# Kernel optimization log

Measured on AMD Instinct MI355X. Metric: run time of the kernel, lower is better.

## Reference

```python
import jax, jax.numpy as jnp
import numpy as np

N_STORE, N_DEPT, F_IN = 100_000, 20_000, 128
E = 1_000_000
H, C = 4, 16  # heads, per-head channels; hidden = H*C = 64
NUM_LAYERS = 3


def setup_inputs() -> dict:
    key = jax.random.key(0)
    ks = jax.random.split(key, 16)
    def edges(k, n_src, n_dst):
        k1, k2 = jax.random.split(k)
        src = jax.random.randint(k1, (E,), 0, n_src, dtype=jnp.int32)
        dst = jax.random.randint(k2, (E,), 0, n_dst, dtype=jnp.int32)
        return jnp.stack([src, dst])
    s = 0.05
    return {
        "x_store": jax.random.normal(ks[0], (N_STORE, F_IN), jnp.float32),
        "x_dept": jax.random.normal(ks[1], (N_DEPT, F_IN), jnp.float32),
        "edge_sd": edges(ks[2], N_STORE, N_DEPT),   # store -> dept
        "edge_ds": edges(ks[3], N_DEPT, N_STORE),   # dept  -> store
        "edge_ss": edges(ks[4], N_STORE, N_STORE),  # store -> store
        "W_src0": jax.random.normal(ks[5], (3, F_IN, H * C), jnp.float32) * s,
        "W_dst0": jax.random.normal(ks[6], (3, F_IN, H * C), jnp.float32) * s,
        "W_src_h": jax.random.normal(ks[7], (2, 3, H * C, H * C), jnp.float32) * s,
        "W_dst_h": jax.random.normal(ks[8], (2, 3, H * C, H * C), jnp.float32) * s,
        "att_src": jax.random.normal(ks[9], (3, 3, H, C), jnp.float32) * s,
        "att_dst": jax.random.normal(ks[10], (3, 3, H, C), jnp.float32) * s,
        "bias": jnp.zeros((3, 3, H * C), jnp.float32),
    }


def gat_conv(x_src, x_dst, edge, W_s, W_d, a_s, a_d, b, n_dst):
    """PyG GATConv, bipartite, add_self_loops=False, eval mode (no dropout)."""
    h_s = (x_src @ W_s).reshape(-1, H, C)   # [N_src, H, C]
    h_d = (x_dst @ W_d).reshape(-1, H, C)   # [N_dst, H, C]
    al_s = jnp.sum(h_s * a_s, axis=-1)      # [N_src, H]
    al_d = jnp.sum(h_d * a_d, axis=-1)      # [N_dst, H]
    src, dst = edge[0], edge[1]
    e = jax.nn.leaky_relu(al_s[src] + al_d[dst], 0.2)        # [E, H]
    m = jax.ops.segment_max(e, dst, num_segments=n_dst)       # segment softmax
    m = jnp.where(jnp.isfinite(m), m, 0.0)
    ex = jnp.exp(e - m[dst])
    denom = jax.ops.segment_sum(ex, dst, num_segments=n_dst)
    alpha = ex / (denom[dst] + 1e-16)                          # [E, H]
    msg = h_s[src] * alpha[:, :, None]                         # [E, H, C]
    out = jax.ops.segment_sum(msg, dst, num_segments=n_dst)    # [N_dst, H, C]
    return out.reshape(n_dst, H * C) + b


def _forward(x_store, x_dept, edge_sd, edge_ds, edge_ss,
             W_src0, W_dst0, W_src_h, W_dst_h, att_src, att_dst, bias):
    xs, xd = x_store, x_dept
    for i in range(NUM_LAYERS):
        Ws = W_src0 if i == 0 else W_src_h[i - 1]
        Wd = W_dst0 if i == 0 else W_dst_h[i - 1]
        # edge type 0: store->dept ; 1: dept->store ; 2: store->store
        o_dept = gat_conv(xs, xd, edge_sd, Ws[0], Wd[0], att_src[i, 0], att_dst[i, 0], bias[i, 0], N_DEPT)
        o1 = gat_conv(xd, xs, edge_ds, Ws[1], Wd[1], att_src[i, 1], att_dst[i, 1], bias[i, 1], N_STORE)
        o2 = gat_conv(xs, xs, edge_ss, Ws[2], Wd[2], att_src[i, 2], att_dst[i, 2], bias[i, 2], N_STORE)
        o_store = (o1 + o2) * 0.5  # HeteroConv aggr='mean' across relations into 'store'
        if i < NUM_LAYERS - 1:
            xs, xd = jax.nn.relu(o_store), jax.nn.relu(o_dept)  # dropout is identity in eval
        else:
            xs, xd = o_store, o_dept
    return jnp.concatenate([xs, xd], axis=0)  # [N_STORE + N_DEPT, 64]


def reference(x_store, x_dept, edge_sd, edge_ds, edge_ss,
              W_src0, W_dst0, W_src_h, W_dst_h, att_src, att_dst, bias):
    return _forward(x_store, x_dept, edge_sd, edge_ds, edge_ss,
                    W_src0, W_dst0, W_src_h, W_dst_h, att_src, att_dst, bias)
```

## Files before the change

kernel.cpp:

```cpp
#include <hip/hip_runtime.h>
#include <hip/hip_bf16.h>

#define N_STORE 100000
#define N_DEPT  20000
#define F_IN    128
#define NTOT    (N_DEPT + 2 * N_STORE)

#define NB0   157
#define NB12  196
#define NBUCK (NB0 + 2 * NB12)

using u16    = unsigned short;
using bf16x8 = __attribute__((ext_vector_type(8))) __bf16;
using f32x4  = __attribute__((ext_vector_type(4))) float;

__device__ __forceinline__ float b2f(u16 x) {
    unsigned u = ((unsigned)x) << 16;
    return __builtin_bit_cast(float, u);
}
__device__ __forceinline__ u16 f2b(float f) {
    unsigned u = __builtin_bit_cast(unsigned, f);
    u += 0x7FFFu + ((u >> 16) & 1u);
    return (u16)(u >> 16);
}

__global__ void k_zeroi(int* p, int n) {
    int i = blockIdx.x * 256 + threadIdx.x;
    if (i < n) p[i] = 0;
}

__global__ void k_bcount(const int* __restrict__ e0, const int* __restrict__ e1,
                         const int* __restrict__ e2, int E, int* __restrict__ bucketCnt) {
    __shared__ int c[256];
    int t = threadIdx.x;
    c[t] = 0; __syncthreads();
    int rel = blockIdx.y;
    const int* e = (rel == 0) ? e0 : (rel == 1) ? e1 : e2;
    int n = (rel == 0) ? N_DEPT : N_STORE;
    int shift = (rel == 0) ? 7 : 9;
    int i0 = blockIdx.x * 2048 + t;
#pragma unroll
    for (int k = 0; k < 8; ++k) {
        int i = i0 + k * 256;
        if (i < E) {
            int d = e[E + i];
            if ((unsigned)d < (unsigned)n) atomicAdd(&c[d >> shift], 1);
        }
    }
    __syncthreads();
    int bbase = (rel == 0) ? 0 : (rel == 1) ? NB0 : NB0 + NB12;
    int nb = (rel == 0) ? NB0 : NB12;
    if (t < nb && c[t]) atomicAdd(&bucketCnt[bbase + t], c[t]);
}

__global__ void k_bscan(const int* __restrict__ bucketCnt, int* __restrict__ bucketOfs,
                        int* __restrict__ bucketCur, int* __restrict__ offs) {
    __shared__ int s[1024];
    int t = threadIdx.x;
    int v = (t < NBUCK) ? bucketCnt[t] : 0;
    s[t] = v; __syncthreads();
    for (int o = 1; o < 1024; o <<= 1) {
        int u = (t >= o) ? s[t - o] : 0;
        __syncthreads();
        s[t] += u;
        __syncthreads();
    }
    if (t < NBUCK) {
        bucketOfs[t + 1] = s[t];
        bucketCur[t] = s[t] - v;
    }
    if (t == 0) bucketOfs[0] = 0;
    if (t == NBUCK - 1) offs[NTOT] = s[t];
}

__global__ void k_bscatter(const int* __restrict__ e0, const int* __restrict__ e1,
                           const int* __restrict__ e2, int E,
                           int* __restrict__ bucketCur, unsigned* __restrict__ pairs) {
    __shared__ int c[256];
    __shared__ int base[256];
    int t = threadIdx.x;
    c[t] = 0; __syncthreads();
    int rel = blockIdx.y;
    const int* e = (rel == 0) ? e0 : (rel == 1) ? e1 : e2;
    int n = (rel == 0) ? N_DEPT : N_STORE;
    int shift = (rel == 0) ? 7 : 9;
    int i0 = blockIdx.x * 2048 + t;
    int mb[8], mr[8]; unsigned mv[8];
#pragma unroll
    for (int k = 0; k < 8; ++k) {
        int i = i0 + k * 256;
        mb[k] = -1;
        if (i < E) {
            int d = e[E + i];
            if ((unsigned)d < (unsigned)n) {
                int b = d >> shift;
                mb[k] = b;
                mr[k] = atomicAdd(&c[b], 1);
                mv[k] = (unsigned)e[i] | ((unsigned)(d - (b << shift)) << 20);
            }
        }
    }
    __syncthreads();
    int bbase = (rel == 0) ? 0 : (rel == 1) ? NB0 : NB0 + NB12;
    int nb = (rel == 0) ? NB0 : NB12;
    if (t < nb && c[t]) base[t] = atomicAdd(&bucketCur[bbase + t], c[t]);
    __syncthreads();
#pragma unroll
    for (int k = 0; k < 8; ++k)
        if (mb[k] >= 0) pairs[base[mb[k]] + mr[k]] = mv[k];
}

__global__ void k_bfinal(const unsigned* __restrict__ pairs, const int* __restrict__ bucketOfs,
                         int* __restrict__ offs, int* __restrict__ srcs_all) {
    int b = blockIdx.x, t = threadIdx.x;
    int rel = (b < NB0) ? 0 : (b < NB0 + NB12) ? 1 : 2;
    int shift = (rel == 0) ? 7 : 9;
    int bLocal = b - ((rel == 0) ? 0 : (rel == 1) ? NB0 : NB0 + NB12);
    int n = (rel == 0) ? N_DEPT : N_STORE;
    int gbase = (rel == 0) ? 0 : (rel == 1) ? N_DEPT : N_DEPT + N_STORE;
    int nodeLo = bLocal << shift;
    int bsize = 1 << shift;
    int nNodes = n - nodeLo; if (nNodes > bsize) nNodes = bsize;
    int pairLo = bucketOfs[b], pairHi = bucketOfs[b + 1];
    __shared__ int cnt[512], sc[512];
    cnt[t] = 0; cnt[t + 256] = 0;
    __syncthreads();
    for (int p = pairLo + t; p < pairHi; p += 256)
        atomicAdd(&cnt[pairs[p] >> 20], 1);
    __syncthreads();
    sc[t] = cnt[t]; sc[t + 256] = cnt[t + 256];
    __syncthreads();
    for (int o = 1; o < 512; o <<= 1) {
        int a0 = (t >= o) ? sc[t - o] : 0;
        int a1 = (t + 256 >= o) ? sc[t + 256 - o] : 0;
        __syncthreads();
        sc[t] += a0; sc[t + 256] += a1;
        __syncthreads();
    }
    int ex0 = sc[t] - cnt[t];
    int ex1 = sc[t + 256] - cnt[t + 256];
    if (t < nNodes)       offs[gbase + nodeLo + t]       = pairLo + ex0;
    if (t + 256 < nNodes) offs[gbase + nodeLo + t + 256] = pairLo + ex1;
    __syncthreads();
    cnt[t] = ex0; cnt[t + 256] = ex1;
    __syncthreads();
    for (int p = pairLo + t; p < pairHi; p += 256) {
        unsigned u = pairs[p];
        int q = atomicAdd(&cnt[u >> 20], 1);
        srcs_all[pairLo + q] = (int)(u & 0xFFFFFu);
    }
}

__global__ void k_pack_store(const float* __restrict__ Wa, const float* __restrict__ Wb,
                             const float* __restrict__ Wd1, const float* __restrict__ Wd2,
                             const float* __restrict__ aS0, const float* __restrict__ aS2,
                             const float* __restrict__ aD1, const float* __restrict__ aD2,
                             int K, u16* __restrict__ out) {
    int id = blockIdx.x * 256 + threadIdx.x;
    int total = K * 144;
    if (id >= total) return;
    int k = id / 144, n = id - k * 144;
    float val;
    if (n < 64) val = Wa[k * 64 + n];
    else if (n < 128) val = Wb[k * 64 + (n - 64)];
    else {
        int g = (n - 128) >> 2, h = (n - 128) & 3;
        const float* W = (g == 0) ? Wa : (g == 1) ? Wb : (g == 2) ? Wd1 : Wd2;
        const float* a = (g == 0) ? aS0 : (g == 1) ? aS2 : (g == 2) ? aD1 : aD2;
        float acc = 0.f;
        for (int c = 0; c < 16; ++c) acc += W[k * 64 + h * 16 + c] * a[h * 16 + c];
        val = acc;
    }
    int KT = K >> 5;
    int ct = n >> 4, col = n & 15, kt = k >> 5, q = (k >> 3) & 3, j = k & 7;
    out[(size_t)((ct * KT + kt) * 64 + q * 16 + col) * 8 + j] = f2b(val);
}

__global__ void k_pack_dept(const float* __restrict__ Ws1, const float* __restrict__ Wd0,
                            const float* __restrict__ aD0, const float* __restrict__ aS1,
                            int K, u16* __restrict__ out) {
    int id = blockIdx.x * 256 + threadIdx.x;
    int total = K * 80;
    if (id >= total) return;
    int k = id / 80, n = id - k * 80;
    float val;
    if (n < 64) val = Ws1[k * 64 + n];
    else if (n < 72) {
        int g = (n - 64) >> 2, h = (n - 64) & 3;
        const float* W = g ? Ws1 : Wd0;
        const float* a = g ? aS1 : aD0;
        float acc = 0.f;
        for (int c = 0; c < 16; ++c) acc += W[k * 64 + h * 16 + c] * a[h * 16 + c];
        val = acc;
    } else val = 0.f;
    int KT = K >> 5;
    int ct = n >> 4, col = n & 15, kt = k >> 5, q = (k >> 3) & 3, j = k & 7;
    out[(size_t)((ct * KT + kt) * 64 + q * 16 + col) * 8 + j] = f2b(val);
}

template <int KT, int CVT, int MODE>
__global__ void k_gemm(const void* __restrict__ Ain, int nrows, int K,
                       const u16* __restrict__ Bpanel,
                       u16* __restrict__ H0, u16* __restrict__ H1,
                       u16* __restrict__ A0, u16* __restrict__ A1, u16* __restrict__ A2) {
    const int CT = (MODE == 0) ? 9 : 5;
    int wid = (blockIdx.x * blockDim.x + threadIdx.x) >> 6;
    int lane = threadIdx.x & 63;
    int m0 = wid << 4;
    if (m0 >= nrows) return;
    int r = lane & 15, q = lane >> 4;
    bf16x8 a[KT];
    if (CVT) {
        const float* ap = (const float*)Ain + (size_t)(m0 + r) * K + q * 8;
#pragma unroll
        for (int kt = 0; kt < KT; ++kt) {
            f32x4 f0 = *(const f32x4*)(ap + kt * 32);
            f32x4 f1 = *(const f32x4*)(ap + kt * 32 + 4);
            bf16x8 v;
#pragma unroll
            for (int j = 0; j < 4; ++j) {
                v[j]     = __builtin_bit_cast(__bf16, f2b(f0[j]));
                v[4 + j] = __builtin_bit_cast(__bf16, f2b(f1[j]));
            }
            a[kt] = v;
        }
    } else {
        const u16* ap = (const u16*)Ain + (size_t)(m0 + r) * K + q * 8;
#pragma unroll
        for (int kt = 0; kt < KT; ++kt) a[kt] = *(const bf16x8*)(ap + kt * 32);
    }
    const bf16x8* B = (const bf16x8*)Bpanel;
    int rowb = m0 + q * 4;
#pragma unroll
    for (int ct = 0; ct < CT; ++ct) {
        f32x4 acc = {0.f, 0.f, 0.f, 0.f};
#pragma unroll
        for (int kt = 0; kt < KT; ++kt)
            acc = __builtin_amdgcn_mfma_f32_16x16x32_bf16(a[kt], B[(ct * KT + kt) * 64 + lane], acc, 0, 0, 0);
        if (ct < 4) {
            u16* cp = H0 + (size_t)rowb * 64 + ct * 16 + r;
#pragma unroll
            for (int i = 0; i < 4; ++i) cp[(size_t)i * 64] = f2b(acc[i]);
        } else if (MODE == 0 && ct < 8) {
            u16* cp = H1 + (size_t)rowb * 64 + (ct - 4) * 16 + r;
#pragma unroll
            for (int i = 0; i < 4; ++i) cp[(size_t)i * 64] = f2b(acc[i]);
        } else {
            if (r < 4) {
                u16* cp = A0 + (size_t)rowb * 4 + r;
#pragma unroll
                for (int i = 0; i < 4; ++i) cp[(size_t)i * 4] = f2b(acc[i]);
            } else if (r < 8) {
                u16* cp = A1 + (size_t)rowb * 4 + (r - 4);
#pragma unroll
                for (int i = 0; i < 4; ++i) cp[(size_t)i * 4] = f2b(acc[i]);
            } else if (MODE == 0) {
                u16* cp = A2 + (size_t)rowb * 8 + (r - 8);
#pragma unroll
                for (int i = 0; i < 4; ++i) cp[(size_t)i * 8] = f2b(acc[i]);
            }
        }
    }
}

__device__ __forceinline__ float warp16_sum(float v) {
    v += __shfl_xor(v, 1);
    v += __shfl_xor(v, 2);
    v += __shfl_xor(v, 4);
    v += __shfl_xor(v, 8);
    return v;
}

__device__ __forceinline__ void agg_seg(const int* __restrict__ srcs, int j0, int j1, int nsrc,
                                        const u16* __restrict__ htab, const u16* __restrict__ altab,
                                        int lane, int slot, int h, int pbase, float ald,
                                        float& acc, float& den) {
    for (int j = j0; j < j1; j += 16) {
        int nb = j1 - j; if (nb > 16) nb = 16;
        int sv = srcs[j + (slot < nb ? slot : 0)];
        sv = ((unsigned)sv < (unsigned)nsrc) ? sv : 0;
        u16 avr = altab[(size_t)sv * 4 + h];
        float hv[16];
#pragma unroll
        for (int k = 0; k < 16; ++k) {
            int s = __builtin_amdgcn_readlane(sv, k);
            hv[k] = b2f(htab[(size_t)s * 64 + lane]);
        }
        float e = b2f(avr) + ald;
        e = (e > 0.f) ? e : 0.2f * e;
        float ex = (slot < nb) ? __expf(e) : 0.f;
        den += ex;
        int exi = __builtin_bit_cast(int, ex);
#pragma unroll
        for (int k = 0; k < 16; ++k) {
            float exv = __builtin_bit_cast(float,
                __builtin_amdgcn_ds_bpermute(pbase + (k << 2), exi));
            acc = fmaf(exv, hv[k], acc);
        }
    }
}

__global__ void __launch_bounds__(256) k_agg1(
                       const int* __restrict__ offs, const int* __restrict__ srcs,
                       const u16* __restrict__ hS0, const u16* __restrict__ alsS0,
                       const u16* __restrict__ aldD0,
                       const float* __restrict__ bias, int doRelu,
                       u16* __restrict__ bOut, float* __restrict__ fOut) {
    __shared__ float sAcc[4][64];
    __shared__ float sDen[4][64];
    int wl = threadIdx.x >> 6;
    int gwid = (blockIdx.x * blockDim.x + threadIdx.x) >> 6;
    int node = gwid >> 1, half = gwid & 1;
    int lane = threadIdx.x & 63, slot = lane & 15, h = lane >> 4;
    int pbase = (lane & 48) << 2;
    float acc = 0.f, den = 0.f;
    bool active = node < N_DEPT;
    if (active) {
        float ald = b2f(aldD0[(size_t)node * 4 + h]);
        int j0 = __builtin_amdgcn_readfirstlane(offs[node]);
        int j1 = __builtin_amdgcn_readfirstlane(offs[node + 1]);
        int cnt = j1 - j0;
        int mid = j0 + (((cnt + 31) >> 5) << 4);
        if (mid > j1) mid = j1;
        int s = half ? mid : j0;
        int e = half ? j1 : mid;
        agg_seg(srcs, s, e, N_STORE, hS0, alsS0, lane, slot, h, pbase, ald, acc, den);
        den = warp16_sum(den);
    }
    sAcc[wl][lane] = acc;
    sDen[wl][lane] = den;
    __syncthreads();
    if (active && half == 0) {
        float accT = acc + sAcc[wl + 1][lane];
        float denT = den + sDen[wl + 1][lane];
        float out = accT / (denT + 1e-16f) + bias[lane];
        if (doRelu) out = out > 0.f ? out : 0.f;
        size_t oi = (size_t)node * 64 + lane;
        if (fOut) fOut[oi] = out;
        else      bOut[oi] = f2b(out);
    }
}

__global__ void k_agg2(const int* __restrict__ offs1, const int* __restrict__ srcs,
                       const int* __restrict__ offs2,
                       const u16* __restrict__ hD, const u16* __restrict__ alsD1,
                       const u16* __restrict__ hS2, const u16* __restrict__ alsS2,
                       const u16* __restrict__ aldS12,
                       const float* __restrict__ bias1, const float* __restrict__ bias2,
                       int doRelu,
                       u16* __restrict__ bOut, float* __restrict__ fOut) {
    int wid = (blockIdx.x * blockDim.x + threadIdx.x) >> 6;
    if (wid >= N_STORE) return;
    int lane = threadIdx.x & 63, slot = lane & 15, h = lane >> 4;
    int pbase = (lane & 48) << 2;
    float ald1 = b2f(aldS12[(size_t)wid * 8 + h]);
    float ald2 = b2f(aldS12[(size_t)wid * 8 + 4 + h]);
    int a0 = __builtin_amdgcn_readfirstlane(offs1[wid]);
    int a1e = __builtin_amdgcn_readfirstlane(offs1[wid + 1]);
    int b0 = __builtin_amdgcn_readfirstlane(offs2[wid]);
    int b1e = __builtin_amdgcn_readfirstlane(offs2[wid + 1]);
    float acc1 = 0.f, den1 = 0.f, acc2 = 0.f, den2 = 0.f;
    agg_seg(srcs, a0, a1e, N_DEPT, hD, alsD1, lane, slot, h, pbase, ald1, acc1, den1);
    agg_seg(srcs, b0, b1e, N_STORE, hS2, alsS2, lane, slot, h, pbase, ald2, acc2, den2);
    den1 = warp16_sum(den1);
    den2 = warp16_sum(den2);
    float out = (acc1 / (den1 + 1e-16f) + bias1[lane] + acc2 / (den2 + 1e-16f) + bias2[lane]) * 0.5f;
    if (doRelu) out = out > 0.f ? out : 0.f;
    size_t oi = (size_t)wid * 64 + lane;
    if (fOut) fOut[oi] = out;
    else      bOut[oi] = f2b(out);
}

extern "C" void kernel_launch(void* const* d_in, const int* in_sizes, int n_in,
                              void* d_out, int out_size, void* d_ws, size_t ws_size,
                              hipStream_t stream) {
    const float* x_store = (const float*)d_in[0];
    const float* x_dept  = (const float*)d_in[1];
    const int* e_sd = (const int*)d_in[2];
    const int* e_ds = (const int*)d_in[3];
    const int* e_ss = (const int*)d_in[4];
    const float* W_src0  = (const float*)d_in[5];
    const float* W_dst0  = (const float*)d_in[6];
    const float* W_src_h = (const float*)d_in[7];
    const float* W_dst_h = (const float*)d_in[8];
    const float* att_src = (const float*)d_in[9];
    const float* att_dst = (const float*)d_in[10];
    const float* bias    = (const float*)d_in[11];
    const int E = in_sizes[2] / 2;

    char* w = (char*)d_ws;
    auto alloc = [&](size_t bytes) -> char* {
        char* p = w;
        w += (bytes + 255) & ~(size_t)255;
        return p;
    };
    int* offs_all  = (int*)alloc((size_t)(NTOT + 1) * 4);
    int* srcs_all  = (int*)alloc((size_t)3 * E * 4);
    int* bucketCnt = (int*)alloc(1024 * 4);
    int* bucketOfs = (int*)alloc(1024 * 4);
    int* bucketCur = (int*)alloc(1024 * 4);
    u16* panelS[3]; u16* panelD[3];
    for (int l = 0; l < 3; ++l) {
        int KT = (l == 0) ? 4 : 2;
        panelS[l] = (u16*)alloc((size_t)KT * 9 * 64 * 8 * 2);
        panelD[l] = (u16*)alloc((size_t)KT * 5 * 64 * 8 * 2);
    }
    u16* hS0    = (u16*)alloc((size_t)N_STORE * 64 * 2);
    u16* hS2    = (u16*)alloc((size_t)N_STORE * 64 * 2);
    u16* hD     = (u16*)alloc((size_t)N_DEPT * 64 * 2);
    u16* alsS0  = (u16*)alloc((size_t)N_STORE * 4 * 2);
    u16* alsS2  = (u16*)alloc((size_t)N_STORE * 4 * 2);
    u16* aldS12 = (u16*)alloc((size_t)N_STORE * 8 * 2);
    u16* aldD0  = (u16*)alloc((size_t)N_DEPT * 4 * 2);
    u16* alsD1  = (u16*)alloc((size_t)N_DEPT * 4 * 2);
    u16* actSA  = (u16*)alloc((size_t)N_STORE * 64 * 2);
    u16* actDA  = (u16*)alloc((size_t)N_DEPT * 64 * 2);
    u16* actSB  = actSA;
    u16* actDB  = actDA;
    unsigned* pairs = (unsigned*)hS0;

    int* off_sd = offs_all;
    int* off_ds = offs_all + N_DEPT;
    int* off_ss = offs_all + N_DEPT + N_STORE;

    float* outStoreF = (float*)d_out;
    float* outDeptF  = outStoreF + (size_t)N_STORE * 64;

    int ebl8 = (E + 2047) / 2048;
    k_zeroi<<<(NBUCK + 255) / 256, 256, 0, stream>>>(bucketCnt, NBUCK);
    k_bcount<<<dim3(ebl8, 3), 256, 0, stream>>>(e_sd, e_ds, e_ss, E, bucketCnt);
    k_bscan<<<1, 1024, 0, stream>>>(bucketCnt, bucketOfs, bucketCur, offs_all);
    k_bscatter<<<dim3(ebl8, 3), 256, 0, stream>>>(e_sd, e_ds, e_ss, E, bucketCur, pairs);
    k_bfinal<<<NBUCK, 256, 0, stream>>>(pairs, bucketOfs, offs_all, srcs_all);

    for (int l = 0; l < 3; ++l) {
        int K = (l == 0) ? 128 : 64;
        const float *Ws[3], *Wd[3], *aS[3], *aD[3];
        for (int rr = 0; rr < 3; ++rr) {
            Ws[rr] = (l == 0) ? W_src0 + (size_t)rr * 128 * 64
                              : W_src_h + (size_t)((l - 1) * 3 + rr) * 64 * 64;
            Wd[rr] = (l == 0) ? W_dst0 + (size_t)rr * 128 * 64
                              : W_dst_h + (size_t)((l - 1) * 3 + rr) * 64 * 64;
            aS[rr] = att_src + (size_t)(l * 3 + rr) * 64;
            aD[rr] = att_dst + (size_t)(l * 3 + rr) * 64;
        }
        k_pack_store<<<(K * 144 + 255) / 256, 256, 0, stream>>>(
            Ws[0], Ws[2], Wd[1], Wd[2], aS[0], aS[2], aD[1], aD[2], K, panelS[l]);
        k_pack_dept<<<(K * 80 + 255) / 256, 256, 0, stream>>>(
            Ws[1], Wd[0], aD[0], aS[1], K, panelD[l]);

        int gbS = (N_STORE / 16 * 64 + 255) / 256;
        int gbD = (N_DEPT / 16 * 64 + 255) / 256;
        if (l == 0) {
            k_gemm<4, 1, 0><<<gbS, 256, 0, stream>>>(x_store, N_STORE, K, panelS[l],
                                                     hS0, hS2, alsS0, alsS2, aldS12);
            k_gemm<4, 1, 1><<<gbD, 256, 0, stream>>>(x_dept, N_DEPT, K, panelD[l],
                                                     hD, nullptr, aldD0, alsD1, nullptr);
        } else if (l == 1) {
            k_gemm<2, 0, 0><<<gbS, 256, 0, stream>>>(actSA, N_STORE, K, panelS[l],
                                                     hS0, hS2, alsS0, alsS2, aldS12);
            k_gemm<2, 0, 1><<<gbD, 256, 0, stream>>>(actDA, N_DEPT, K, panelD[l],
                                                     hD, nullptr, aldD0, alsD1, nullptr);
        } else {
            k_gemm<2, 0, 0><<<gbS, 256, 0, stream>>>(actSB, N_STORE, K, panelS[l],
                                                     hS0, hS2, alsS0, alsS2, aldS12);
            k_gemm<2, 0, 1><<<gbD, 256, 0, stream>>>(actDB, N_DEPT, K, panelD[l],
                                                     hD, nullptr, aldD0, alsD1, nullptr);
        }

        int relu = (l < 2) ? 1 : 0;
        u16* bS = (l == 0) ? actSA : actSB;
        u16* bD = (l == 0) ? actDA : actDB;
        float* fS = (l == 2) ? outStoreF : nullptr;
        float* fD = (l == 2) ? outDeptF  : nullptr;
        k_agg1<<<N_DEPT / 2, 256, 0, stream>>>(
            off_sd, srcs_all, hS0, alsS0, aldD0,
            bias + (size_t)(l * 3 + 0) * 64, relu, bD, fD);
        k_agg2<<<N_STORE / 4, 256, 0, stream>>>(
            off_ds, srcs_all, off_ss,
            hD, alsD1, hS2, alsS2, aldS12,
            bias + (size_t)(l * 3 + 1) * 64, bias + (size_t)(l * 3 + 2) * 64,
            relu, bS, fS);
    }
    (void)n_in; (void)out_size; (void)ws_size;
}
```

Before: 566.2 us.

## Gather 4 channels per lane with 8-byte loads in GAT aggregation

The edge aggregation now assigns each lane 4 channels of one of 4 source rows at a time, loading 8 bytes per lane instead of 2 bytes for each of 16 rows. Each lane's partial sums are then reduced across the four row groups with shuffles, and a quarter of the wave writes vectorised outputs. The aim is fewer, wider gather instructions and fewer bpermutes per 16-edge chunk. In exchange it adds cross-lane reduction work, leaves 48 of 64 lanes idle during the output phase, and removes the node<N_DEPT guard in k_agg1, which relies on the grid size matching exactly.

```diff
diff --git a/kernel.cpp b/kernel.cpp
--- a/kernel.cpp
+++ b/kernel.cpp
@@ -11,6 +11,8 @@
 #define NBUCK (NB0 + 2 * NB12)
 
 using u16    = unsigned short;
+using u16x4  = __attribute__((ext_vector_type(4))) unsigned short;
+using u32x2  = __attribute__((ext_vector_type(2))) unsigned;
 using bf16x8 = __attribute__((ext_vector_type(8))) __bf16;
 using f32x4  = __attribute__((ext_vector_type(4))) float;
 
@@ -273,30 +275,50 @@
 
 __device__ __forceinline__ void agg_seg(const int* __restrict__ srcs, int j0, int j1, int nsrc,
                                         const u16* __restrict__ htab, const u16* __restrict__ altab,
-                                        int lane, int slot, int h, int pbase, float ald,
-                                        float& acc, float& den) {
+                                        int slot, int h, int qoff, int cexo, int choff,
+                                        float ald, f32x4& acc, float& den) {
     for (int j = j0; j < j1; j += 16) {
         int nb = j1 - j; if (nb > 16) nb = 16;
         int sv = srcs[j + (slot < nb ? slot : 0)];
         sv = ((unsigned)sv < (unsigned)nsrc) ? sv : 0;
         u16 avr = altab[(size_t)sv * 4 + h];
-        float hv[16];
-#pragma unroll
-        for (int k = 0; k < 16; ++k) {
-            int s = __builtin_amdgcn_readlane(sv, k);
-            hv[k] = b2f(htab[(size_t)s * 64 + lane]);
-        }
         float e = b2f(avr) + ald;
         e = (e > 0.f) ? e : 0.2f * e;
         float ex = (slot < nb) ? __expf(e) : 0.f;
         den += ex;
         int exi = __builtin_bit_cast(int, ex);
-#pragma unroll
-        for (int k = 0; k < 16; ++k) {
-            float exv = __builtin_bit_cast(float,
-                __builtin_amdgcn_ds_bpermute(pbase + (k << 2), exi));
-            acc = fmaf(exv, hv[k], acc);
-        }
+        int rowv[4];
+#pragma unroll
+        for (int k = 0; k < 4; ++k)
+            if (4 * k < nb)
+                rowv[k] = __builtin_amdgcn_ds_bpermute(qoff + (k << 4), sv);
+        u32x2 dv[4];
+#pragma unroll
+        for (int k = 0; k < 4; ++k)
+            if (4 * k < nb)
+                dv[k] = *(const u32x2*)(htab + ((size_t)(unsigned)rowv[k] << 6) + choff);
+        float exv[4];
+#pragma unroll
+        for (int k = 0; k < 4; ++k)
+            if (4 * k < nb)
+                exv[k] = __builtin_bit_cast(float,
+                    __builtin_amdgcn_ds_bpermute(qoff + cexo + (k << 4), exi));
+#pragma unroll
+        for (int k = 0; k < 4; ++k)
+            if (4 * k < nb) {
+                acc[0] = fmaf(exv[k], __builtin_bit_cast(float, dv[k][0] << 16), acc[0]);
+                acc[1] = fmaf(exv[k], __builtin_bit_cast(float, dv[k][0] & 0xFFFF0000u), acc[1]);
+                acc[2] = fmaf(exv[k], __builtin_bit_cast(float, dv[k][1] << 16), acc[2]);
+                acc[3] = fmaf(exv[k], __builtin_bit_cast(float, dv[k][1] & 0xFFFF0000u), acc[3]);
+            }
+    }
+}
+
+__device__ __forceinline__ void quad_reduce(f32x4& a) {
+#pragma unroll
+    for (int i = 0; i < 4; ++i) {
+        a[i] += __shfl_xor(a[i], 16);
+        a[i] += __shfl_xor(a[i], 32);
     }
 }
 
@@ -306,38 +328,49 @@
                        const u16* __restrict__ aldD0,
                        const float* __restrict__ bias, int doRelu,
                        u16* __restrict__ bOut, float* __restrict__ fOut) {
-    __shared__ float sAcc[4][64];
+    __shared__ f32x4 sAcc[4][64];
     __shared__ float sDen[4][64];
     int wl = threadIdx.x >> 6;
     int gwid = (blockIdx.x * blockDim.x + threadIdx.x) >> 6;
     int node = gwid >> 1, half = gwid & 1;
     int lane = threadIdx.x & 63, slot = lane & 15, h = lane >> 4;
-    int pbase = (lane & 48) << 2;
-    float acc = 0.f, den = 0.f;
-    bool active = node < N_DEPT;
-    if (active) {
-        float ald = b2f(aldD0[(size_t)node * 4 + h]);
-        int j0 = __builtin_amdgcn_readfirstlane(offs[node]);
-        int j1 = __builtin_amdgcn_readfirstlane(offs[node + 1]);
-        int cnt = j1 - j0;
-        int mid = j0 + (((cnt + 31) >> 5) << 4);
-        if (mid > j1) mid = j1;
-        int s = half ? mid : j0;
-        int e = half ? j1 : mid;
-        agg_seg(srcs, s, e, N_STORE, hS0, alsS0, lane, slot, h, pbase, ald, acc, den);
-        den = warp16_sum(den);
-    }
+    int qoff = h << 2;
+    int cexo = (slot >> 2) << 6;
+    int choff = slot << 2;
+    f32x4 acc = {0.f, 0.f, 0.f, 0.f};
+    float den = 0.f;
+    float ald = b2f(aldD0[(size_t)node * 4 + h]);
+    int j0 = __builtin_amdgcn_readfirstlane(offs[node]);
+    int j1 = __builtin_amdgcn_readfirstlane(offs[node + 1]);
+    int cnt = j1 - j0;
+    int mid = j0 + (((cnt + 31) >> 5) << 4);
+    if (mid > j1) mid = j1;
+    int s = half ? mid : j0;
+    int e = half ? j1 : mid;
+    agg_seg(srcs, s, e, N_STORE, hS0, alsS0, slot, h, qoff, cexo, choff, ald, acc, den);
+    den = warp16_sum(den);
+    quad_reduce(acc);
+    float dOwn = __shfl(den, (slot >> 2) << 4);
     sAcc[wl][lane] = acc;
     sDen[wl][lane] = den;
     __syncthreads();
-    if (active && half == 0) {
-        float accT = acc + sAcc[wl + 1][lane];
-        float denT = den + sDen[wl + 1][lane];
-        float out = accT / (denT + 1e-16f) + bias[lane];
-        if (doRelu) out = out > 0.f ? out : 0.f;
-        size_t oi = (size_t)node * 64 + lane;
-        if (fOut) fOut[oi] = out;
-        else      bOut[oi] = f2b(out);
+    if (half == 0 && lane < 16) {
+        f32x4 accO = sAcc[wl + 1][lane];
+        float dT = dOwn + sDen[wl + 1][(slot >> 2) << 4];
+        f32x4 b4 = ((const f32x4*)bias)[slot];
+        f32x4 o;
+#pragma unroll
+        for (int i = 0; i < 4; ++i) {
+            float v = (acc[i] + accO[i]) / (dT + 1e-16f) + b4[i];
+            o[i] = doRelu ? (v > 0.f ? v : 0.f) : v;
+        }
+        if (fOut) ((f32x4*)fOut)[(size_t)node * 16 + slot] = o;
+        else {
+            u16x4 p;
+#pragma unroll
+            for (int i = 0; i < 4; ++i) p[i] = f2b(o[i]);
+            ((u16x4*)bOut)[(size_t)node * 16 + slot] = p;
+        }
     }
 }
 
@@ -352,23 +385,43 @@
     int wid = (blockIdx.x * blockDim.x + threadIdx.x) >> 6;
     if (wid >= N_STORE) return;
     int lane = threadIdx.x & 63, slot = lane & 15, h = lane >> 4;
-    int pbase = (lane & 48) << 2;
+    int qoff = h << 2;
+    int cexo = (slot >> 2) << 6;
+    int choff = slot << 2;
     float ald1 = b2f(aldS12[(size_t)wid * 8 + h]);
     float ald2 = b2f(aldS12[(size_t)wid * 8 + 4 + h]);
     int a0 = __builtin_amdgcn_readfirstlane(offs1[wid]);
     int a1e = __builtin_amdgcn_readfirstlane(offs1[wid + 1]);
     int b0 = __builtin_amdgcn_readfirstlane(offs2[wid]);
     int b1e = __builtin_amdgcn_readfirstlane(offs2[wid + 1]);
-    float acc1 = 0.f, den1 = 0.f, acc2 = 0.f, den2 = 0.f;
-    agg_seg(srcs, a0, a1e, N_DEPT, hD, alsD1, lane, slot, h, pbase, ald1, acc1, den1);
-    agg_seg(srcs, b0, b1e, N_STORE, hS2, alsS2, lane, slot, h, pbase, ald2, acc2, den2);
+    f32x4 acc1 = {0.f, 0.f, 0.f, 0.f}, acc2 = {0.f, 0.f, 0.f, 0.f};
+    float den1 = 0.f, den2 = 0.f;
+    agg_seg(srcs, a0, a1e, N_DEPT, hD, alsD1, slot, h, qoff, cexo, choff, ald1, acc1, den1);
+    agg_seg(srcs, b0, b1e, N_STORE, hS2, alsS2, slot, h, qoff, cexo, choff, ald2, acc2, den2);
     den1 = warp16_sum(den1);
     den2 = warp16_sum(den2);
-    float out = (acc1 / (den1 + 1e-16f) + bias1[lane] + acc2 / (den2 + 1e-16f) + bias2[lane]) * 0.5f;
-    if (doRelu) out = out > 0.f ? out : 0.f;
-    size_t oi = (size_t)wid * 64 + lane;
-    if (fOut) fOut[oi] = out;
-    else      bOut[oi] = f2b(out);
+    quad_reduce(acc1);
+    quad_reduce(acc2);
+    int denLane = (slot >> 2) << 4;
+    float d1 = __shfl(den1, denLane);
+    float d2 = __shfl(den2, denLane);
+    if (lane < 16) {
+        f32x4 b1 = ((const f32x4*)bias1)[slot];
+        f32x4 b2 = ((const f32x4*)bias2)[slot];
+        f32x4 o;
+#pragma unroll
+        for (int i = 0; i < 4; ++i) {
+            float v = (acc1[i] / (d1 + 1e-16f) + b1[i] + acc2[i] / (d2 + 1e-16f) + b2[i]) * 0.5f;
+            o[i] = doRelu ? (v > 0.f ? v : 0.f) : v;
+        }
+        if (fOut) ((f32x4*)fOut)[(size_t)wid * 16 + slot] = o;
+        else {
+            u16x4 p;
+#pragma unroll
+            for (int i = 0; i < 4; ++i) p[i] = f2b(o[i]);
+            ((u16x4*)bOut)[(size_t)wid * 16 + slot] = p;
+        }
+    }
 }
 
 extern "C" void kernel_launch(void* const* d_in, const int* in_sizes, int n_in,
```

Result: no change. 562.6 us (-0.6%).
